# Performance work log

Measured on AMD Instinct MI355X. Metric: run time of the kernel, lower is better.

Reference implementation:

```python
import jax, jax.numpy as jnp
import numpy as np

N_IN, C, T, E, N_OUT, F = 50000, 64, 8, 800000, 50000, 64


def setup_inputs() -> dict:
    key = jax.random.key(0)
    k0, k1, k2, k3, k4 = jax.random.split(key, 5)
    node_features = jax.random.normal(k0, (N_IN, C), dtype=jnp.float32)
    edge_features = jax.random.normal(k1, (T, E), dtype=jnp.float32)
    idx_out = jax.random.randint(k2, (E,), 0, N_OUT)
    idx_in = jax.random.randint(k3, (E,), 0, N_IN)
    indices = jnp.stack([idx_out, idx_in], axis=1).astype(jnp.int64)  # [E, 2]
    # glorot-ish scale for kernel [T, C, F]
    scale = np.sqrt(2.0 / (C + F)).astype(np.float32)
    kernel = jax.random.normal(k4, (T, C, F), dtype=jnp.float32) * scale
    bias = jnp.zeros((F,), dtype=jnp.float32)
    return {
        "node_features": node_features,
        "edge_features": edge_features,
        "indices": indices,
        "kernel": kernel,
        "bias": bias,
        "out_size": N_OUT,
    }


def reference(node_features, edge_features, indices, kernel, bias, out_size):
    # sparse_conv (combine='unstack'):
    #   out[i] = sum_t ( segment_sum_{e: out(e)=i} ef[t,e] * x[in(e)] ) @ kernel[t] + bias
    gathered = node_features[indices[:, 1]]          # [E, C] irregular gather
    seg_ids = indices[:, 0]
    n_terms = kernel.shape[0]                        # small fixed structural dim
    out = jnp.zeros((out_size, kernel.shape[2]), dtype=node_features.dtype)
    for t in range(n_terms):
        weighted = edge_features[t][:, None] * gathered            # [E, C]
        agg = jax.ops.segment_sum(weighted, seg_ids, num_segments=out_size)  # [No, C]
        out = out + agg @ kernel[t]                                # [No, F]
    return out + bias
```

## Files before the change

### kernel.cpp

```cpp
#include <hip/hip_runtime.h>

constexpr int N_IN  = 50000;
constexpr int C     = 64;
constexpr int T     = 8;
constexpr int E     = 800000;
constexpr int N_OUT = 50000;
constexpr int F     = 64;

constexpr int BINSZ     = 2048;
constexpr int NBIN      = (E + BINSZ - 1) / BINSZ;
constexpr int CHUNK     = 4096;
constexpr int BP_BLOCKS = (E + CHUNK - 1) / CHUNK;

constexpr size_t OFF_NFBF = 0;
constexpr size_t OFF_KT   = 6400000;
constexpr size_t OFF_CNT  = OFF_KT + 65536;
constexpr size_t OFF_BSUM = OFF_CNT + 200064;
constexpr size_t OFF_BCUR = OFF_BSUM + 1024;
constexpr size_t OFF_RANK = OFF_BCUR + 2048;
constexpr size_t OFF_EFT  = OFF_RANK + 3200000;
constexpr size_t OFF_BPRM = OFF_EFT + 25600000;
constexpr size_t OFF_ISRT = OFF_BPRM + 6400000;
constexpr size_t OFF_EPRM = OFF_ISRT + 3200000;
static_assert(OFF_EFT % 16 == 0 && OFF_BPRM % 8 == 0, "alignment");

typedef __attribute__((ext_vector_type(8))) short short8;
typedef __attribute__((ext_vector_type(4))) float f32x4;

__device__ inline unsigned short f2bf(float x) {
    unsigned int u = __float_as_uint(x);
    unsigned int r = (u + 0x7FFFu + ((u >> 16) & 1u)) >> 16;
    return (unsigned short)r;
}
__device__ inline float bf2f(unsigned short u) {
    return __uint_as_float(((unsigned int)u) << 16);
}

constexpr int NF_BLOCKS   = N_IN * C / 4 / 256;
constexpr int KT_BLOCKS   = 32;
constexpr int ET_BLOCKS   = E / 256;
constexpr int HIST_BLOCKS = E / 256;

__global__ __launch_bounds__(256) void prep_kernel(const float* __restrict__ nf,
                                                   const float* __restrict__ Kmat,
                                                   const float* __restrict__ ef,
                                                   const int* __restrict__ idx,
                                                   unsigned short* __restrict__ nf_bf,
                                                   unsigned short* __restrict__ K_T,
                                                   float* __restrict__ ef_T,
                                                   int* __restrict__ cnt,
                                                   int* __restrict__ rank) {
    const int b   = blockIdx.x;
    const int tid = threadIdx.x;

    if (b < NF_BLOCKS) {
        int i = b * 256 + tid;
        float4 v = ((const float4*)nf)[i];
        unsigned int u0 = (unsigned int)f2bf(v.x) | ((unsigned int)f2bf(v.y) << 16);
        unsigned int u1 = (unsigned int)f2bf(v.z) | ((unsigned int)f2bf(v.w) << 16);
        ((uint2*)nf_bf)[i] = make_uint2(u0, u1);
    } else if (b < NF_BLOCKS + KT_BLOCKS) {
        for (int k = (b - NF_BLOCKS) * 256 + tid; k < T * C * F; k += KT_BLOCKS * 256) {
            int f = k & 63;
            int c = (k >> 6) & 63;
            int t = k >> 12;
            K_T[f * 512 + t * 64 + c] = f2bf(Kmat[k]);
        }
    } else if (b < NF_BLOCKS + KT_BLOCKS + ET_BLOCKS) {
        int e = (b - NF_BLOCKS - KT_BLOCKS) * 256 + tid;
        float w[8];
#pragma unroll
        for (int t = 0; t < T; ++t) w[t] = ef[(size_t)t * E + e];
        float4* dst = (float4*)(ef_T + (size_t)e * 8);
        dst[0] = make_float4(w[0], w[1], w[2], w[3]);
        dst[1] = make_float4(w[4], w[5], w[6], w[7]);
    } else {
        int e = (b - NF_BLOCKS - KT_BLOCKS - ET_BLOCKS) * 256 + tid;
        int o = idx[2 * e];
        rank[e] = atomicAdd(&cnt[o], 1);
    }
}

__global__ __launch_bounds__(256) void scanA_kernel(int* __restrict__ cnt,
                                                    int* __restrict__ bsum) {
    __shared__ int sh[256];
    const int tid = threadIdx.x;
    int g = blockIdx.x * 256 + tid;
    int v = (g < N_OUT) ? cnt[g] : 0;
    sh[tid] = v;
    __syncthreads();
#pragma unroll
    for (int off = 1; off < 256; off <<= 1) {
        int x = 0;
        if (tid >= off) x = sh[tid - off];
        __syncthreads();
        if (tid >= off) sh[tid] += x;
        __syncthreads();
    }
    int incl = sh[tid];
    if (g < N_OUT) cnt[g] = incl - v;
    if (tid == 255) bsum[blockIdx.x] = incl;
}

__global__ __launch_bounds__(256) void scanBC_kernel(int* __restrict__ cnt,
                                                     const int* __restrict__ bsum,
                                                     int* __restrict__ bincur) {
    __shared__ int sh[256];
    const int bi  = blockIdx.x;
    const int tid = threadIdx.x;
    sh[tid] = (tid < bi) ? bsum[tid] : 0;
    __syncthreads();
#pragma unroll
    for (int off = 128; off >= 1; off >>= 1) {
        if (tid < off) sh[tid] += sh[tid + off];
        __syncthreads();
    }
    const int offset = sh[0];
    int g = bi * 256 + tid;
    if (g < N_OUT) cnt[g] = cnt[g] + offset;
    if (bi == 0) {
        if (tid == 0) cnt[N_OUT] = E;
        for (int g2 = tid; g2 < NBIN; g2 += 256) bincur[g2] = g2 * BINSZ;
    }
}

__global__ __launch_bounds__(256) void buildperm_kernel(const int* __restrict__ idx,
                                                        const int* __restrict__ rank,
                                                        const int* __restrict__ start,
                                                        int* __restrict__ bincur,
                                                        uint2* __restrict__ binperm) {
    __shared__ int hist[NBIN];
    __shared__ int lcnt[NBIN];
    __shared__ int gdel[NBIN];
    __shared__ int sc[512];
    __shared__ uint2 stage[CHUNK];
    __shared__ int gpos[CHUNK];

    const int tid = threadIdx.x;
    const int e0  = blockIdx.x * CHUNK;

    for (int b = tid; b < NBIN; b += 256) { hist[b] = 0; lcnt[b] = 0; }
    __syncthreads();

    int pos_r[16], in_r[16];
#pragma unroll
    for (int k = 0; k < 16; ++k) {
        int e = e0 + k * 256 + tid;
        pos_r[k] = -1;
        if (e < E) {
            int2 oi = ((const int2*)idx)[e];
            int p = start[oi.x] + rank[e];
            pos_r[k] = p;
            in_r[k]  = oi.y;
            atomicAdd(&hist[p >> 11], 1);
        }
    }
    __syncthreads();

    sc[tid]       = (tid < NBIN) ? hist[tid] : 0;
    sc[tid + 256] = (tid + 256 < NBIN) ? hist[tid + 256] : 0;
    __syncthreads();
    for (int off = 1; off < 512; off <<= 1) {
        int a0 = sc[tid], a1 = sc[tid + 256];
        int b0 = (tid >= off) ? sc[tid - off] : 0;
        int b1 = (tid + 256 >= off) ? sc[tid + 256 - off] : 0;
        __syncthreads();
        sc[tid] = a0 + b0;
        sc[tid + 256] = a1 + b1;
        __syncthreads();
    }

    for (int b = tid; b < NBIN; b += 256) {
        int c = hist[b];
        if (c > 0) gdel[b] = atomicAdd(&bincur[b], c);
    }
    __syncthreads();

#pragma unroll
    for (int k = 0; k < 16; ++k) {
        if (pos_r[k] >= 0) {
            int e  = e0 + k * 256 + tid;
            int p  = pos_r[k];
            int b  = p >> 11;
            int lr = atomicAdd(&lcnt[b], 1);
            int lbase = (b == 0) ? 0 : sc[b - 1];
            int li = lbase + lr;
            stage[li] = make_uint2(((unsigned)(p & (BINSZ - 1)) << 20) | (unsigned)e,
                                   (unsigned)in_r[k]);
            gpos[li] = gdel[b] + lr;
        }
    }
    __syncthreads();

    const int tot = sc[NBIN - 1];
    for (int i = tid; i < tot; i += 256)
        binperm[gpos[i]] = stage[i];
}

__global__ __launch_bounds__(256) void permfix_kernel(const uint2* __restrict__ binperm,
                                                      int* __restrict__ isorted,
                                                      int* __restrict__ eperm) {
    const int base = blockIdx.x * BINSZ;
    const int n = min(BINSZ, E - base);
    for (int i = threadIdx.x; i < n; i += 256) {
        uint2 u = binperm[base + i];
        int off = (int)(u.x >> 20);
        int e   = (int)(u.x & 0xFFFFFu);
        isorted[base + off] = (int)u.y;
        eperm[base + off]   = e;
    }
}

__global__ __launch_bounds__(256) void aggregate_kernel(const unsigned short* __restrict__ nf_bf,
                                                        const unsigned short* __restrict__ K_T,
                                                        const int* __restrict__ start,
                                                        const int* __restrict__ isorted,
                                                        const int* __restrict__ eperm,
                                                        const float* __restrict__ ef_T,
                                                        const float* __restrict__ bias,
                                                        float* __restrict__ out) {
    __shared__ unsigned short A_lds[16][520];

    const int wave = threadIdx.x >> 6;
    const int lane = threadIdx.x & 63;
    const int node_base = blockIdx.x * 16;

    for (int q = 0; q < 4; ++q) {
        const int m = wave * 4 + q;
        const int o = node_base + m;
        const int s0 = __builtin_amdgcn_readfirstlane(start[o]);
        const int s1 = __builtin_amdgcn_readfirstlane(start[o + 1]);

        float acc[8] = {0.f, 0.f, 0.f, 0.f, 0.f, 0.f, 0.f, 0.f};

        for (int base = s0; base < s1; base += 64) {
            const int cnt = min(64, s1 - base);
            int iv = (base + lane < s1) ? isorted[base + lane] : 0;
            int ev = (base + lane < s1) ? eperm[base + lane] : 0;

            int j = 0;
            for (; j + 4 <= cnt; j += 4) {
                const int i0 = __builtin_amdgcn_readlane(iv, j + 0);
                const int i1 = __builtin_amdgcn_readlane(iv, j + 1);
                const int i2 = __builtin_amdgcn_readlane(iv, j + 2);
                const int i3 = __builtin_amdgcn_readlane(iv, j + 3);
                float x0 = bf2f(nf_bf[(size_t)i0 * 64 + lane]);
                float x1 = bf2f(nf_bf[(size_t)i1 * 64 + lane]);
                float x2 = bf2f(nf_bf[(size_t)i2 * 64 + lane]);
                float x3 = bf2f(nf_bf[(size_t)i3 * 64 + lane]);
                const float* w0 = ef_T + (size_t)__builtin_amdgcn_readlane(ev, j + 0) * 8;
                const float* w1 = ef_T + (size_t)__builtin_amdgcn_readlane(ev, j + 1) * 8;
                const float* w2 = ef_T + (size_t)__builtin_amdgcn_readlane(ev, j + 2) * 8;
                const float* w3 = ef_T + (size_t)__builtin_amdgcn_readlane(ev, j + 3) * 8;
#pragma unroll
                for (int t = 0; t < T; ++t) {
                    acc[t] += w0[t] * x0;
                    acc[t] += w1[t] * x1;
                    acc[t] += w2[t] * x2;
                    acc[t] += w3[t] * x3;
                }
            }
            for (; j < cnt; ++j) {
                const int i0 = __builtin_amdgcn_readlane(iv, j);
                float x0 = bf2f(nf_bf[(size_t)i0 * 64 + lane]);
                const float* w0 = ef_T + (size_t)__builtin_amdgcn_readlane(ev, j) * 8;
#pragma unroll
                for (int t = 0; t < T; ++t) acc[t] += w0[t] * x0;
            }
        }

#pragma unroll
        for (int t = 0; t < T; ++t) A_lds[m][t * 64 + lane] = f2bf(acc[t]);
    }
    __syncthreads();

    const int mrow = lane & 15;
    const int kb   = lane >> 4;
    const int fcol = wave * 16 + mrow;

    f32x4 acc4 = {0.f, 0.f, 0.f, 0.f};
#pragma unroll
    for (int s = 0; s < 16; ++s) {
        const int k0 = s * 32 + kb * 8;
        short8 a = *(const short8*)&A_lds[mrow][k0];
        short8 b = *(const short8*)(K_T + (size_t)fcol * 512 + k0);
        acc4 = __builtin_amdgcn_mfma_f32_16x16x32_bf16(a, b, acc4, 0, 0, 0);
    }

    const float bv = bias[fcol];
#pragma unroll
    for (int r = 0; r < 4; ++r) {
        const int m = kb * 4 + r;
        out[(size_t)(node_base + m) * F + fcol] = acc4[r] + bv;
    }
}

extern "C" void kernel_launch(void* const* d_in, const int* in_sizes, int n_in,
                              void* d_out, int out_size, void* d_ws, size_t ws_size,
                              hipStream_t stream) {
    const float* nf   = (const float*)d_in[0];
    const float* ef   = (const float*)d_in[1];
    const int*   idx  = (const int*)d_in[2];
    const float* Kmat = (const float*)d_in[3];
    const float* bias = (const float*)d_in[4];
    float*       out  = (float*)d_out;

    char* ws = (char*)d_ws;
    unsigned short* nf_bf   = (unsigned short*)(ws + OFF_NFBF);
    unsigned short* K_T     = (unsigned short*)(ws + OFF_KT);
    int*            cnt     = (int*)(ws + OFF_CNT);
    int*            bsum    = (int*)(ws + OFF_BSUM);
    int*            bincur  = (int*)(ws + OFF_BCUR);
    int*            rank    = (int*)(ws + OFF_RANK);
    float*          ef_T    = (float*)(ws + OFF_EFT);
    uint2*          binperm = (uint2*)(ws + OFF_BPRM);
    int*            isorted = (int*)(ws + OFF_ISRT);
    int*            eperm   = (int*)(ws + OFF_EPRM);

    const int nchunks = (N_OUT + 255) / 256;

    hipMemsetAsync(cnt, 0, (N_OUT + 1) * sizeof(int), stream);
    prep_kernel<<<NF_BLOCKS + KT_BLOCKS + ET_BLOCKS + HIST_BLOCKS, 256, 0, stream>>>(
        nf, Kmat, ef, idx, nf_bf, K_T, ef_T, cnt, rank);
    scanA_kernel<<<nchunks, 256, 0, stream>>>(cnt, bsum);
    scanBC_kernel<<<nchunks, 256, 0, stream>>>(cnt, bsum, bincur);
    buildperm_kernel<<<BP_BLOCKS, 256, 0, stream>>>(idx, rank, cnt, bincur, binperm);
    permfix_kernel<<<NBIN, 256, 0, stream>>>(binperm, isorted, eperm);
    aggregate_kernel<<<N_OUT / 16, 256, 0, stream>>>(
        nf_bf, K_T, cnt, isorted, eperm, ef_T, bias, out);
}
```

Baseline: 222.0 us.

## Carry edge weights through the sort to make aggregate weight reads contiguous

Drops the separate edge-feature transpose and the edge permutation array. Instead, buildperm writes each edge's 8 weights into its bin slot, and permfix scatters them into destination-sorted order alongside the input index. The aggregate kernel then reads weights sequentially through a wave-uniform pointer instead of gathering them by edge id. The cost is an extra 25.6 MB intermediate buffer and an additional write/read pass over the weights. The bin entry packs the in-node index into 16 bits, which only holds because N_IN is below 65536.

```diff
diff --git a/kernel.cpp b/kernel.cpp
--- a/kernel.cpp
+++ b/kernel.cpp
@@ -18,11 +18,11 @@
 constexpr size_t OFF_BSUM = OFF_CNT + 200064;
 constexpr size_t OFF_BCUR = OFF_BSUM + 1024;
 constexpr size_t OFF_RANK = OFF_BCUR + 2048;
-constexpr size_t OFF_EFT  = OFF_RANK + 3200000;
-constexpr size_t OFF_BPRM = OFF_EFT + 25600000;
-constexpr size_t OFF_ISRT = OFF_BPRM + 6400000;
-constexpr size_t OFF_EPRM = OFF_ISRT + 3200000;
-static_assert(OFF_EFT % 16 == 0 && OFF_BPRM % 8 == 0, "alignment");
+constexpr size_t OFF_BENT = OFF_RANK + 3200000;
+constexpr size_t OFF_BNW  = OFF_BENT + 3200000;
+constexpr size_t OFF_ISRT = OFF_BNW + 25600000;
+constexpr size_t OFF_WSRT = OFF_ISRT + 3200000;
+static_assert(OFF_BNW % 16 == 0 && OFF_WSRT % 16 == 0, "f32x4 alignment");
 
 typedef __attribute__((ext_vector_type(8))) short short8;
 typedef __attribute__((ext_vector_type(4))) float f32x4;
@@ -38,16 +38,13 @@
 
 constexpr int NF_BLOCKS   = N_IN * C / 4 / 256;
 constexpr int KT_BLOCKS   = 32;
-constexpr int ET_BLOCKS   = E / 256;
 constexpr int HIST_BLOCKS = E / 256;
 
 __global__ __launch_bounds__(256) void prep_kernel(const float* __restrict__ nf,
                                                    const float* __restrict__ Kmat,
-                                                   const float* __restrict__ ef,
                                                    const int* __restrict__ idx,
                                                    unsigned short* __restrict__ nf_bf,
                                                    unsigned short* __restrict__ K_T,
-                                                   float* __restrict__ ef_T,
                                                    int* __restrict__ cnt,
                                                    int* __restrict__ rank) {
     const int b   = blockIdx.x;
@@ -66,16 +63,8 @@
             int t = k >> 12;
             K_T[f * 512 + t * 64 + c] = f2bf(Kmat[k]);
         }
-    } else if (b < NF_BLOCKS + KT_BLOCKS + ET_BLOCKS) {
+    } else {
         int e = (b - NF_BLOCKS - KT_BLOCKS) * 256 + tid;
-        float w[8];
-#pragma unroll
-        for (int t = 0; t < T; ++t) w[t] = ef[(size_t)t * E + e];
-        float4* dst = (float4*)(ef_T + (size_t)e * 8);
-        dst[0] = make_float4(w[0], w[1], w[2], w[3]);
-        dst[1] = make_float4(w[4], w[5], w[6], w[7]);
-    } else {
-        int e = (b - NF_BLOCKS - KT_BLOCKS - ET_BLOCKS) * 256 + tid;
         int o = idx[2 * e];
         rank[e] = atomicAdd(&cnt[o], 1);
     }
@@ -127,13 +116,15 @@
 __global__ __launch_bounds__(256) void buildperm_kernel(const int* __restrict__ idx,
                                                         const int* __restrict__ rank,
                                                         const int* __restrict__ start,
+                                                        const float* __restrict__ ef,
                                                         int* __restrict__ bincur,
-                                                        uint2* __restrict__ binperm) {
+                                                        unsigned* __restrict__ binent,
+                                                        float* __restrict__ binw) {
     __shared__ int hist[NBIN];
     __shared__ int lcnt[NBIN];
     __shared__ int gdel[NBIN];
     __shared__ int sc[512];
-    __shared__ uint2 stage[CHUNK];
+    __shared__ unsigned stage[CHUNK];
     __shared__ int gpos[CHUNK];
 
     const int tid = threadIdx.x;
@@ -176,38 +167,58 @@
     }
     __syncthreads();
 
+    int gp_r[16];
 #pragma unroll
     for (int k = 0; k < 16; ++k) {
         if (pos_r[k] >= 0) {
-            int e  = e0 + k * 256 + tid;
             int p  = pos_r[k];
             int b  = p >> 11;
             int lr = atomicAdd(&lcnt[b], 1);
             int lbase = (b == 0) ? 0 : sc[b - 1];
             int li = lbase + lr;
-            stage[li] = make_uint2(((unsigned)(p & (BINSZ - 1)) << 20) | (unsigned)e,
-                                   (unsigned)in_r[k]);
-            gpos[li] = gdel[b] + lr;
+            stage[li] = ((unsigned)(p & (BINSZ - 1)) << 16) | (unsigned)in_r[k];
+            int g = gdel[b] + lr;
+            gpos[li] = g;
+            gp_r[k]  = g;
         }
     }
     __syncthreads();
 
     const int tot = sc[NBIN - 1];
     for (int i = tid; i < tot; i += 256)
-        binperm[gpos[i]] = stage[i];
-}
-
-__global__ __launch_bounds__(256) void permfix_kernel(const uint2* __restrict__ binperm,
+        binent[gpos[i]] = stage[i];
+
+#pragma unroll
+    for (int k = 0; k < 16; ++k) {
+        if (pos_r[k] >= 0) {
+            int e = e0 + k * 256 + tid;
+            float w[8];
+#pragma unroll
+            for (int t = 0; t < T; ++t) w[t] = ef[(size_t)t * E + e];
+            float4* dst = (float4*)(binw + (size_t)gp_r[k] * 8);
+            dst[0] = make_float4(w[0], w[1], w[2], w[3]);
+            dst[1] = make_float4(w[4], w[5], w[6], w[7]);
+        }
+    }
+}
+
+__global__ __launch_bounds__(256) void permfix_kernel(const unsigned* __restrict__ binent,
+                                                      const float* __restrict__ binw,
                                                       int* __restrict__ isorted,
-                                                      int* __restrict__ eperm) {
+                                                      float* __restrict__ wsorted) {
     const int base = blockIdx.x * BINSZ;
     const int n = min(BINSZ, E - base);
     for (int i = threadIdx.x; i < n; i += 256) {
-        uint2 u = binperm[base + i];
-        int off = (int)(u.x >> 20);
-        int e   = (int)(u.x & 0xFFFFFu);
-        isorted[base + off] = (int)u.y;
-        eperm[base + off]   = e;
+        unsigned u = binent[base + i];
+        int off = (int)(u >> 16);
+        int in  = (int)(u & 0xFFFFu);
+        const float4* src = (const float4*)(binw + (size_t)(base + i) * 8);
+        float4 w0 = src[0];
+        float4 w1 = src[1];
+        isorted[base + off] = in;
+        float4* dst = (float4*)(wsorted + (size_t)(base + off) * 8);
+        dst[0] = w0;
+        dst[1] = w1;
     }
 }
 
@@ -215,8 +226,7 @@
                                                         const unsigned short* __restrict__ K_T,
                                                         const int* __restrict__ start,
                                                         const int* __restrict__ isorted,
-                                                        const int* __restrict__ eperm,
-                                                        const float* __restrict__ ef_T,
+                                                        const float* __restrict__ wsorted,
                                                         const float* __restrict__ bias,
                                                         float* __restrict__ out) {
     __shared__ unsigned short A_lds[16][520];
@@ -236,7 +246,6 @@
         for (int base = s0; base < s1; base += 64) {
             const int cnt = min(64, s1 - base);
             int iv = (base + lane < s1) ? isorted[base + lane] : 0;
-            int ev = (base + lane < s1) ? eperm[base + lane] : 0;
 
             int j = 0;
             for (; j + 4 <= cnt; j += 4) {
@@ -248,24 +257,23 @@
                 float x1 = bf2f(nf_bf[(size_t)i1 * 64 + lane]);
                 float x2 = bf2f(nf_bf[(size_t)i2 * 64 + lane]);
                 float x3 = bf2f(nf_bf[(size_t)i3 * 64 + lane]);
-                const float* w0 = ef_T + (size_t)__builtin_amdgcn_readlane(ev, j + 0) * 8;
-                const float* w1 = ef_T + (size_t)__builtin_amdgcn_readlane(ev, j + 1) * 8;
-                const float* w2 = ef_T + (size_t)__builtin_amdgcn_readlane(ev, j + 2) * 8;
-                const float* w3 = ef_T + (size_t)__builtin_amdgcn_readlane(ev, j + 3) * 8;
+                const float* wp = wsorted +
+                    (size_t)__builtin_amdgcn_readfirstlane(base + j) * 8;
 #pragma unroll
                 for (int t = 0; t < T; ++t) {
-                    acc[t] += w0[t] * x0;
-                    acc[t] += w1[t] * x1;
-                    acc[t] += w2[t] * x2;
-                    acc[t] += w3[t] * x3;
+                    acc[t] += wp[t] * x0;
+                    acc[t] += wp[8 + t] * x1;
+                    acc[t] += wp[16 + t] * x2;
+                    acc[t] += wp[24 + t] * x3;
                 }
             }
             for (; j < cnt; ++j) {
                 const int i0 = __builtin_amdgcn_readlane(iv, j);
                 float x0 = bf2f(nf_bf[(size_t)i0 * 64 + lane]);
-                const float* w0 = ef_T + (size_t)__builtin_amdgcn_readlane(ev, j) * 8;
-#pragma unroll
-                for (int t = 0; t < T; ++t) acc[t] += w0[t] * x0;
+                const float* wp = wsorted +
+                    (size_t)__builtin_amdgcn_readfirstlane(base + j) * 8;
+#pragma unroll
+                for (int t = 0; t < T; ++t) acc[t] += wp[t] * x0;
             }
         }
 
@@ -312,20 +320,21 @@
     int*            bsum    = (int*)(ws + OFF_BSUM);
     int*            bincur  = (int*)(ws + OFF_BCUR);
     int*            rank    = (int*)(ws + OFF_RANK);
-    float*          ef_T    = (float*)(ws + OFF_EFT);
-    uint2*          binperm = (uint2*)(ws + OFF_BPRM);
+    unsigned*       binent  = (unsigned*)(ws + OFF_BENT);
+    float*          binw    = (float*)(ws + OFF_BNW);
     int*            isorted = (int*)(ws + OFF_ISRT);
-    int*            eperm   = (int*)(ws + OFF_EPRM);
+    float*          wsorted = (float*)(ws + OFF_WSRT);
 
     const int nchunks = (N_OUT + 255) / 256;
 
     hipMemsetAsync(cnt, 0, (N_OUT + 1) * sizeof(int), stream);
-    prep_kernel<<<NF_BLOCKS + KT_BLOCKS + ET_BLOCKS + HIST_BLOCKS, 256, 0, stream>>>(
-        nf, Kmat, ef, idx, nf_bf, K_T, ef_T, cnt, rank);
+    prep_kernel<<<NF_BLOCKS + KT_BLOCKS + HIST_BLOCKS, 256, 0, stream>>>(
+        nf, Kmat, idx, nf_bf, K_T, cnt, rank);
     scanA_kernel<<<nchunks, 256, 0, stream>>>(cnt, bsum);
     scanBC_kernel<<<nchunks, 256, 0, stream>>>(cnt, bsum, bincur);
-    buildperm_kernel<<<BP_BLOCKS, 256, 0, stream>>>(idx, rank, cnt, bincur, binperm);
-    permfix_kernel<<<NBIN, 256, 0, stream>>>(binperm, isorted, eperm);
+    buildperm_kernel<<<BP_BLOCKS, 256, 0, stream>>>(idx, rank, cnt, ef, bincur,
+                                                    binent, binw);
+    permfix_kernel<<<NBIN, 256, 0, stream>>>(binent, binw, isorted, wsorted);
     aggregate_kernel<<<N_OUT / 16, 256, 0, stream>>>(
-        nf_bf, K_T, cnt, isorted, eperm, ef_T, bias, out);
-}
+        nf_bf, K_T, cnt, isorted, wsorted, bias, out);
+}
```

New measurement: 242.3 us. +9.1%, slower.
